# Performance work log

Hardware: AMD Instinct MI355X
Metric: run time of the kernel (lower is better)

## Reference

```python
import jax, jax.numpy as jnp
import numpy as np


def setup_inputs() -> dict:
    key = jax.random.key(0)
    k1, k2, k3, k4, k5 = jax.random.split(key, 5)
    B, T, H, E, F = 4, 2048, 2048, 8, 1024
    s_h = 1.0 / np.sqrt(H)
    s_f = 1.0 / np.sqrt(F)
    return {
        "hidden_states": jax.random.normal(k1, (B, T, H), dtype=jnp.float32),
        "W_router": jax.random.normal(k2, (H, E), dtype=jnp.float32) * s_h,
        "W_gate": jax.random.normal(k3, (E, H, F), dtype=jnp.float32) * s_h,
        "W_up": jax.random.normal(k4, (E, H, F), dtype=jnp.float32) * s_h,
        "W_down": jax.random.normal(k5, (E, F, H), dtype=jnp.float32) * s_f,
    }


def reference(hidden_states, W_router, W_gate, W_up, W_down):
    B, T, H = hidden_states.shape
    E = W_router.shape[1]
    x = hidden_states.reshape(-1, H)  # [N, H]
    # ReMoE router: linear -> ReLU, non-negative weights per expert
    weights = jax.nn.relu(x @ W_router)  # [N, E]
    # Per-expert SwiGLU FFN applied to all tokens; zero-weight experts
    # contribute exactly zero, matching the original masked dispatch.
    gate = jnp.einsum('nh,ehf->enf', x, W_gate)  # [E, N, F]
    up = jnp.einsum('nh,ehf->enf', x, W_up)      # [E, N, F]
    hid = jax.nn.silu(gate) * up                 # [E, N, F]
    expert_out = jnp.einsum('enf,efh->enh', hid, W_down)  # [E, N, H]
    out_flat = jnp.einsum('ne,enh->nh', weights, expert_out)  # [N, H]
    out = out_flat.reshape(B, T, H)
    router_weights = weights.reshape(B, T, E)
    return (out, router_weights)
```

## Files before the change

### kernel.cpp

```cpp
#include <hip/hip_runtime.h>
#include <hip/hip_bf16.h>

#define N_TOK 8192
#define HD    2048
#define NE    8
#define FF    1024

using f32x4  = __attribute__((ext_vector_type(4))) float;
using bf16x8 = __attribute__((ext_vector_type(8))) __bf16;

__device__ __forceinline__ unsigned short f2bf(float f) {
  unsigned u = __float_as_uint(f);
  u += 0x7FFFu + ((u >> 16) & 1u);
  return (unsigned short)(u >> 16);
}

__device__ __forceinline__ void gl_lds16(const void* g, void* l) {
  __builtin_amdgcn_global_load_lds((__attribute__((address_space(1))) void*)g,
                                   (__attribute__((address_space(3))) void*)l,
                                   16, 0, 0);
}

#define WAIT8_BAR() do {                                      \
    asm volatile("s_waitcnt vmcnt(8)" ::: "memory");          \
    __builtin_amdgcn_s_barrier();                             \
    __builtin_amdgcn_sched_barrier(0);                        \
  } while (0)

__global__ void k_tconv(const float* __restrict__ in, unsigned short* __restrict__ out,
                        int R, int C, size_t in_z, size_t out_z, size_t ostride) {
  __shared__ float tile[32][33];
  const int z = blockIdx.z;
  const int c0 = blockIdx.x * 32, r0 = blockIdx.y * 32;
  const int tx = threadIdx.x, ty = threadIdx.y;
  const float* ip = in + (size_t)z * in_z;
  unsigned short* op = out + (size_t)z * out_z;
  #pragma unroll
  for (int i = ty; i < 32; i += 8)
    tile[i][tx] = ip[(size_t)(r0 + i) * C + (c0 + tx)];
  __syncthreads();
  #pragma unroll
  for (int i = ty; i < 32; i += 8)
    op[(size_t)(c0 + i) * ostride + (r0 + tx)] = f2bf(tile[tx][i]);
}

__global__ void k_router(const float* __restrict__ x, const float* __restrict__ Wr,
                         float* __restrict__ w, float* __restrict__ rout,
                         unsigned short* __restrict__ xb) {
  const int lane = threadIdx.x & 63, wv = threadIdx.x >> 6;
  const int n = blockIdx.x * 4 + wv;
  const float* xr = x + (size_t)n * HD + lane * 32;
  unsigned short* xbr = xb + (size_t)n * HD + lane * 32;
  const float* wbase = Wr + (size_t)lane * 32 * NE;
  float acc[8];
  #pragma unroll
  for (int e = 0; e < 8; ++e) acc[e] = 0.f;
  #pragma unroll
  for (int kk = 0; kk < 32; kk += 4) {
    float4 xv = *reinterpret_cast<const float4*>(xr + kk);
    ushort4 o;
    o.x = f2bf(xv.x); o.y = f2bf(xv.y); o.z = f2bf(xv.z); o.w = f2bf(xv.w);
    *reinterpret_cast<ushort4*>(xbr + kk) = o;
    #pragma unroll
    for (int t = 0; t < 4; ++t) {
      const float* wrow = wbase + (kk + t) * 8;
      float4 w0 = *reinterpret_cast<const float4*>(wrow);
      float4 w1 = *reinterpret_cast<const float4*>(wrow + 4);
      float xs = (t == 0) ? xv.x : (t == 1) ? xv.y : (t == 2) ? xv.z : xv.w;
      acc[0] += xs * w0.x; acc[1] += xs * w0.y; acc[2] += xs * w0.z; acc[3] += xs * w0.w;
      acc[4] += xs * w1.x; acc[5] += xs * w1.y; acc[6] += xs * w1.z; acc[7] += xs * w1.w;
    }
  }
  #pragma unroll
  for (int off = 32; off; off >>= 1) {
    #pragma unroll
    for (int e = 0; e < 8; ++e) acc[e] += __shfl_down(acc[e], off);
  }
  if (lane == 0) {
    #pragma unroll
    for (int e = 0; e < 8; ++e) {
      float v = acc[e] > 0.f ? acc[e] : 0.f;
      w[n * 8 + e] = v;
      rout[n * 8 + e] = v;
    }
  }
}

__global__ void k_compact(const float* __restrict__ w, int* __restrict__ idx,
                          int* __restrict__ cnt) {
  const int e = blockIdx.x;
  __shared__ int base;
  __shared__ int scan[4];
  if (threadIdx.x == 0) base = 0;
  __syncthreads();
  const int lane = threadIdx.x & 63, wvi = threadIdx.x >> 6;
  for (int c0 = 0; c0 < N_TOK; c0 += 256) {
    const int n = c0 + threadIdx.x;
    const bool act = w[n * 8 + e] > 0.f;
    unsigned long long m = __ballot(act);
    const int pre  = __popcll(m & ((1ull << lane) - 1ull));
    if (lane == 0) scan[wvi] = __popcll(m);
    __syncthreads();
    int woff = 0;
    #pragma unroll
    for (int i = 0; i < 4; ++i) if (i < wvi) woff += scan[i];
    const int tot = scan[0] + scan[1] + scan[2] + scan[3];
    if (act) idx[e * N_TOK + base + woff + pre] = n;
    __syncthreads();
    if (threadIdx.x == 0) base += tot;
    __syncthreads();
  }
  const int M = base;
  if (threadIdx.x == 0) cnt[e] = M;
  const int Mpad = (M + 255) & ~255;
  for (int i = M + threadIdx.x; i < Mpad; i += 256) idx[e * N_TOK + i] = 0;
}

#define G1_MFMA(accM, barr) do {                                                 \
    __builtin_amdgcn_s_setprio(1);                                               \
    _Pragma("unroll")                                                            \
    for (int i = 0; i < 4; ++i) {                                                \
      _Pragma("unroll")                                                          \
      for (int j = 0; j < 4; ++j)                                                \
        accM[i][j] = __builtin_amdgcn_mfma_f32_16x16x32_bf16(av_[i], (barr)[j], accM[i][j], 0,0,0); \
    }                                                                            \
    __builtin_amdgcn_s_setprio(0);                                               \
  } while (0)

#define G1_ST_A(koff, base) do {                                                 \
    gl_lds16(aP0 + (koff), (base) + wv * 1024);                                  \
    gl_lds16(aP1 + (koff), (base) + (wv + 8) * 1024);                            \
  } while (0)
#define G1_ST_B(koff, bgb, bub) do {                                             \
    gl_lds16(gBg + bOff + (koff), (bgb) + wv * 1024);                            \
    gl_lds16(gBu + bOff + (koff), (bub) + wv * 1024);                            \
  } while (0)

#define G1_HALF(rsl, hh, ISSUE_B) do {                                           \
    const char* Ab_ = As  + (rsl) * 32768 + (hh) * 16384 + aoff;                 \
    const char* Bg_ = Bgs + (rsl) * 16384 + (hh) * 8192 + boff;                  \
    const char* Bu_ = Bus + (rsl) * 16384 + (hh) * 8192 + boff;                  \
    bf16x8 av_[4], bb_[4];                                                       \
    _Pragma("unroll")                                                            \
    for (int i = 0; i < 4; ++i) av_[i] = *(const bf16x8*)(Ab_ + i * 1024);       \
    _Pragma("unroll")                                                            \
    for (int j = 0; j < 4; ++j) bb_[j] = *(const bf16x8*)(Bg_ + j * 1024);       \
    G1_MFMA(ag, bb_);                                                            \
    ISSUE_B;                                                                     \
    _Pragma("unroll")                                                            \
    for (int j = 0; j < 4; ++j) bb_[j] = *(const bf16x8*)(Bu_ + j * 1024);       \
    G1_MFMA(au, bb_);                                                            \
  } while (0)

__global__ void __launch_bounds__(512, 2) k_gemm1(
    const unsigned short* __restrict__ xb,
    const unsigned short* __restrict__ Wg,
    const unsigned short* __restrict__ Wu,
    const float* __restrict__ w,
    const int* __restrict__ idx,
    const int* __restrict__ cnt,
    unsigned short* __restrict__ A2,
    int e0, int k2g, int nwg) {
  extern __shared__ char lds[];
  char* As  = lds;
  char* Bgs = lds + 65536;
  char* Bus = lds + 98304;
  const int tid = threadIdx.x;
  const int l = tid & 63, wv = tid >> 6;

  const int h = blockIdx.x;
  const int chunk = nwg >> 3;
  const int L = (h & 7) * chunk + (h >> 3);
  const int eloc = L >> 8;
  const int e = e0 + eloc;
  const int idxq = L & 255;
  const int sub = idxq >> 5;
  const int f = ((sub & 1) << 2) | ((idxq >> 3) & 3);
  const int y = ((sub >> 1) << 3) | (idxq & 7);
  const int bm = y << 8;
  const int bf = f << 7;
  const int wr = wv >> 1, wc = wv & 1;

  const int Me = cnt[e];
  if (bm >= Me) return;
  const int* idxe = idx + e * N_TOK;

  const unsigned short* gBg = Wg + ((size_t)e * FF + bf) * HD;
  const unsigned short* gBu = Wu + ((size_t)e * FF + bf) * HD;

  const int scolE = (((l & 3) ^ ((l >> 3) & 3)) << 3);
  const int fr  = l & 15;
  const int cph = (((l >> 4) ^ ((fr >> 1) & 3)) << 4);
  const int aoff = (wr * 64 + fr) * 64 + cph;
  const int boff = (wc * 64 + fr) * 64 + cph;

  const unsigned short* aP0 = xb + (size_t)idxe[bm + wv * 16 + (l >> 2)] * HD + scolE;
  const unsigned short* aP1 = xb + (size_t)idxe[bm + (wv + 8) * 16 + (l >> 2)] * HD + scolE;
  const size_t bOff = (size_t)(wv * 16 + (l >> 2)) * HD + scolE;

  f32x4 ag[4][4], au[4][4];
  const f32x4 zero = {0.f, 0.f, 0.f, 0.f};
  #pragma unroll
  for (int i = 0; i < 4; ++i) {
    #pragma unroll
    for (int j = 0; j < 4; ++j) { ag[i][j] = zero; au[i][j] = zero; }
  }

  G1_ST_A(0,  As);
  G1_ST_B(0,  Bgs, Bus);
  G1_ST_A(32, As + 16384);
  G1_ST_B(32, Bgs + 8192, Bus + 8192);
  G1_ST_A(64, As + 32768);
  G1_ST_B(64, Bgs + 16384, Bus + 16384);
  WAIT8_BAR();

  const int NT = HD / 64;
  for (int t = 0; t < NT; ++t) {
    const int rs = t & 1, sw = rs ^ 1;
    const int kn1 = ((t + 1 < NT) ? t + 1 : NT - 1) * 64;
    const int kn2 = ((t + 2 < NT) ? t + 2 : NT - 1) * 64;
    G1_ST_A(kn1 + 32, As + sw * 32768 + 16384);
    G1_HALF(rs, 0, G1_ST_B(kn1 + 32, Bgs + sw * 16384 + 8192, Bus + sw * 16384 + 8192));
    WAIT8_BAR();
    G1_ST_A(kn2, As + rs * 32768);
    G1_HALF(rs, 1, G1_ST_B(kn2, Bgs + rs * 16384, Bus + rs * 16384));
    WAIT8_BAR();
  }

  const int orow = (l >> 4) << 2;
  #pragma unroll
  for (int am = 0; am < 4; ++am) {
    #pragma unroll
    for (int rr = 0; rr < 4; ++rr) {
      const int cm = bm + wr * 64 + am * 16 + orow + rr;
      const int n = idxe[cm];
      const float wn = w[n * 8 + e];
      size_t obase = (size_t)n * k2g + (size_t)eloc * FF + bf + wc * 64 + fr;
      #pragma unroll
      for (int j = 0; j < 4; ++j) {
        const float g = ag[am][j][rr];
        const float u = au[am][j][rr];
        const float s = g / (1.f + __expf(-g));
        A2[obase + j * 16] = f2bf(s * u * wn);
      }
    }
  }
}

#define G2_ST_A(koff, base) do {                                                 \
    gl_lds16(gA + aOff0 + (koff), (base) + wv * 1024);                           \
    gl_lds16(gA + aOff1 + (koff), (base) + (wv + 8) * 1024);                     \
  } while (0)
#define G2_ST_B(koff, base) do {                                                 \
    gl_lds16(gB + bOff0 + (koff), (base) + wv * 1024);                           \
    gl_lds16(gB + bOff1 + (koff), (base) + (wv + 8) * 1024);                     \
  } while (0)

#define G2_HALF(rsl, hh, ISSUE_B) do {                                           \
    const char* Ab_ = As + (rsl) * 32768 + (hh) * 16384 + aoff;                  \
    const char* Bb_ = Bs + (rsl) * 32768 + (hh) * 16384 + boff;                  \
    bf16x8 av_[8], bv_[4];                                                       \
    _Pragma("unroll")                                                            \
    for (int i = 0; i < 8; ++i) av_[i] = *(const bf16x8*)(Ab_ + i * 1024);       \
    _Pragma("unroll")                                                            \
    for (int j = 0; j < 4; ++j) bv_[j] = *(const bf16x8*)(Bb_ + j * 1024);       \
    __builtin_amdgcn_s_setprio(1);                                               \
    _Pragma("unroll")                                                            \
    for (int i = 0; i < 4; ++i) {                                                \
      _Pragma("unroll")                                                          \
      for (int j = 0; j < 4; ++j)                                                \
        acc[i][j] = __builtin_amdgcn_mfma_f32_16x16x32_bf16(av_[i], bv_[j], acc[i][j], 0,0,0); \
    }                                                                            \
    __builtin_amdgcn_s_setprio(0);                                               \
    ISSUE_B;                                                                     \
    __builtin_amdgcn_s_setprio(1);                                               \
    _Pragma("unroll")                                                            \
    for (int i = 4; i < 8; ++i) {                                                \
      _Pragma("unroll")                                                          \
      for (int j = 0; j < 4; ++j)                                                \
        acc[i][j] = __builtin_amdgcn_mfma_f32_16x16x32_bf16(av_[i], bv_[j], acc[i][j], 0,0,0); \
    }                                                                            \
    __builtin_amdgcn_s_setprio(0);                                               \
  } while (0)

__global__ void __launch_bounds__(512, 2) k_gemm2(
    const unsigned short* __restrict__ A2,
    const unsigned short* __restrict__ Wd,
    float* __restrict__ out,
    int k2g, int accum) {
  extern __shared__ char lds[];
  char* As = lds;
  char* Bs = lds + 65536;
  const int tid = threadIdx.x;
  const int l = tid & 63, wv = tid >> 6;

  const int h = blockIdx.x;
  const int L = (h & 7) * 32 + (h >> 3);
  const int y = L >> 3;
  const int x = L & 7;
  const int bm = y << 8;
  const int bn = x << 8;
  const int wr = wv >> 2, wc = wv & 3;

  const unsigned short* gA = A2 + (size_t)bm * k2g;
  const unsigned short* gB = Wd + (size_t)bn * (NE * FF);

  const int scolE = (((l & 3) ^ ((l >> 3) & 3)) << 3);
  const int fr  = l & 15;
  const int cph = (((l >> 4) ^ ((fr >> 1) & 3)) << 4);
  const int aoff = (wr * 128 + fr) * 64 + cph;
  const int boff = (wc * 64 + fr) * 64 + cph;

  const size_t aOff0 = (size_t)(wv * 16 + (l >> 2)) * k2g + scolE;
  const size_t aOff1 = (size_t)((wv + 8) * 16 + (l >> 2)) * k2g + scolE;
  const size_t bOff0 = (size_t)(wv * 16 + (l >> 2)) * (NE * FF) + scolE;
  const size_t bOff1 = (size_t)((wv + 8) * 16 + (l >> 2)) * (NE * FF) + scolE;

  f32x4 acc[8][4];
  const f32x4 zero = {0.f, 0.f, 0.f, 0.f};
  #pragma unroll
  for (int i = 0; i < 8; ++i) {
    #pragma unroll
    for (int j = 0; j < 4; ++j) acc[i][j] = zero;
  }

  G2_ST_A(0,  As);
  G2_ST_B(0,  Bs);
  G2_ST_A(32, As + 16384);
  G2_ST_B(32, Bs + 16384);
  G2_ST_A(64, As + 32768);
  G2_ST_B(64, Bs + 32768);
  WAIT8_BAR();

  const int NT = k2g / 64;
  for (int t = 0; t < NT; ++t) {
    const int rs = t & 1, sw = rs ^ 1;
    const int kn1 = ((t + 1 < NT) ? t + 1 : NT - 1) * 64;
    const int kn2 = ((t + 2 < NT) ? t + 2 : NT - 1) * 64;
    G2_ST_A(kn1 + 32, As + sw * 32768 + 16384);
    G2_HALF(rs, 0, G2_ST_B(kn1 + 32, Bs + sw * 32768 + 16384));
    WAIT8_BAR();
    G2_ST_A(kn2, As + rs * 32768);
    G2_HALF(rs, 1, G2_ST_B(kn2, Bs + rs * 32768));
    WAIT8_BAR();
  }

  const int orow = (l >> 4) << 2;
  #pragma unroll
  for (int am = 0; am < 8; ++am) {
    #pragma unroll
    for (int rr = 0; rr < 4; ++rr) {
      const int n = bm + wr * 128 + am * 16 + orow + rr;
      float* op = out + (size_t)n * HD + bn + wc * 64 + fr;
      #pragma unroll
      for (int j = 0; j < 4; ++j) {
        const float v = acc[am][j][rr];
        op[j * 16] = accum ? (op[j * 16] + v) : v;
      }
    }
  }
}

extern "C" void kernel_launch(void* const* d_in, const int* in_sizes, int n_in,
                              void* d_out, int out_size, void* d_ws, size_t ws_size,
                              hipStream_t stream) {
  (void)in_sizes; (void)out_size;
  if (n_in < 5) return;
  const float* x  = (const float*)d_in[0];
  const float* Wr = (const float*)d_in[1];
  const float* Wg = (const float*)d_in[2];
  const float* Wu = (const float*)d_in[3];
  const float* Wd = (const float*)d_in[4];
  float* out  = (float*)d_out;
  float* rout = out + (size_t)N_TOK * HD;

  hipFuncSetAttribute((const void*)k_gemm1, hipFuncAttributeMaxDynamicSharedMemorySize, 131072);
  hipFuncSetAttribute((const void*)k_gemm2, hipFuncAttributeMaxDynamicSharedMemorySize, 131072);

  char* ws = (char*)d_ws;
  const size_t SZ_XB = (size_t)N_TOK * HD * 2;
  const size_t SZ_W  = (size_t)NE * HD * FF * 2;
  unsigned short* xb    = (unsigned short*)(ws);
  unsigned short* Wg_bt = (unsigned short*)(ws + SZ_XB);
  unsigned short* Wu_bt = (unsigned short*)(ws + SZ_XB + SZ_W);
  unsigned short* Wd_bt = (unsigned short*)(ws + SZ_XB + 2 * SZ_W);
  float*          wbuf  = (float*)(ws + SZ_XB + 3 * SZ_W);
  size_t off = SZ_XB + 3 * SZ_W + (size_t)N_TOK * NE * 4;
  int* idxbuf = (int*)(ws + off);  off += (size_t)NE * N_TOK * 4;
  int* cntbuf = (int*)(ws + off);  off += 256;
  const size_t fixed = off;
  unsigned short* A2 = (unsigned short*)(ws + fixed);

  const size_t perE = (size_t)N_TOK * FF * 2;
  int G = 8;
  while (G > 1 && fixed + (size_t)G * perE > ws_size) G >>= 1;

  dim3 tb(32, 8);
  k_tconv<<<dim3(FF / 32, HD / 32, NE), tb, 0, stream>>>(
      Wg, Wg_bt, HD, FF, (size_t)HD * FF, (size_t)FF * HD, (size_t)HD);
  k_tconv<<<dim3(FF / 32, HD / 32, NE), tb, 0, stream>>>(
      Wu, Wu_bt, HD, FF, (size_t)HD * FF, (size_t)FF * HD, (size_t)HD);
  k_tconv<<<dim3(HD / 32, FF / 32, NE), tb, 0, stream>>>(
      Wd, Wd_bt, FF, HD, (size_t)FF * HD, (size_t)FF, (size_t)(NE * FF));

  k_router<<<N_TOK / 4, 256, 0, stream>>>(x, Wr, wbuf, rout, xb);

  k_compact<<<NE, 256, 0, stream>>>(wbuf, idxbuf, cntbuf);

  const int k2g = G * FF;
  for (int e0 = 0; e0 < NE; e0 += G) {
    hipMemsetAsync(A2, 0, (size_t)G * perE, stream);
    const int nwg1 = 256 * G;
    k_gemm1<<<nwg1, 512, 131072, stream>>>(xb, Wg_bt, Wu_bt, wbuf, idxbuf, cntbuf,
                                           A2, e0, k2g, nwg1);
    k_gemm2<<<(N_TOK / 256) * (HD / 256), 512, 131072, stream>>>(
        A2, Wd_bt + (size_t)e0 * FF, out, k2g, e0 != 0);
  }
}
```

Before: 710.3 us.

## Restructure GEMM main loops into 8-phase ping-pong schedule with wave-contiguous LDS staging

Both expert GEMM kernels move from a 3-stage prefetch with half-tile compute to a double-buffered loop split into four phases per K tile. Each phase reads one operand slice from LDS, issues the next global-to-LDS copies, then synchronises and runs a 16-MFMA block. Staging addresses now map each thread to a contiguous tid*16 slot rather than per-wave rows. The aim is to interleave LDS reads, global loads and MFMA work more finely, in the style of ping-pong scheduling. The cost is more barriers per tile and one fewer stage of prefetch depth.

```diff
diff --git a/kernel.cpp b/kernel.cpp
--- a/kernel.cpp
+++ b/kernel.cpp
@@ -9,6 +9,16 @@
 using f32x4  = __attribute__((ext_vector_type(4))) float;
 using bf16x8 = __attribute__((ext_vector_type(8))) __bf16;
 
+#define MFMA16(a, b, c) __builtin_amdgcn_mfma_f32_16x16x32_bf16((a), (b), (c), 0, 0, 0)
+#define BARX() do { __builtin_amdgcn_s_barrier(); __builtin_amdgcn_sched_barrier(0); } while (0)
+#define PH_BAR() do {                                           \
+    __builtin_amdgcn_sched_barrier(0);                          \
+    __builtin_amdgcn_s_barrier();                               \
+    asm volatile("s_waitcnt lgkmcnt(0)" ::: "memory");          \
+    __builtin_amdgcn_sched_barrier(0);                          \
+  } while (0)
+#define VMW4() asm volatile("s_waitcnt vmcnt(4)" ::: "memory")
+
 __device__ __forceinline__ unsigned short f2bf(float f) {
   unsigned u = __float_as_uint(f);
   u += 0x7FFFu + ((u >> 16) & 1u);
@@ -20,12 +30,6 @@
                                    (__attribute__((address_space(3))) void*)l,
                                    16, 0, 0);
 }
-
-#define WAIT8_BAR() do {                                      \
-    asm volatile("s_waitcnt vmcnt(8)" ::: "memory");          \
-    __builtin_amdgcn_s_barrier();                             \
-    __builtin_amdgcn_sched_barrier(0);                        \
-  } while (0)
 
 __global__ void k_tconv(const float* __restrict__ in, unsigned short* __restrict__ out,
                         int R, int C, size_t in_z, size_t out_z, size_t ostride) {
@@ -116,40 +120,33 @@
   for (int i = M + threadIdx.x; i < Mpad; i += 256) idx[e * N_TOK + i] = 0;
 }
 
-#define G1_MFMA(accM, barr) do {                                                 \
+#define G1_STA(kb, kh, d) do {                                                   \
+    gl_lds16(aPs0 + (kb) + (kh) * 32, As + (d) * 32768 + (kh) * 16384 + tid * 16);          \
+    gl_lds16(aPs1 + (kb) + (kh) * 32, As + (d) * 32768 + (kh) * 16384 + 8192 + tid * 16);   \
+  } while (0)
+#define G1_STB(kb, kh, d) do {                                                   \
+    gl_lds16(gBgs + (kb) + (kh) * 32, Bgs + (d) * 16384 + (kh) * 8192 + tid * 16);          \
+    gl_lds16(gBus + (kb) + (kh) * 32, Bus + (d) * 16384 + (kh) * 8192 + tid * 16);          \
+  } while (0)
+#define G1_RDA(kh) do {                                                          \
+    const char* p_ = As + d * 32768 + (kh) * 16384 + arow + cphR;                \
+    av[0] = *(const bf16x8*)(p_);        av[1] = *(const bf16x8*)(p_ + 1024);    \
+    av[2] = *(const bf16x8*)(p_ + 2048); av[3] = *(const bf16x8*)(p_ + 3072);    \
+  } while (0)
+#define G1_RDB(B_, kh) do {                                                      \
+    const char* p_ = (B_) + d * 16384 + (kh) * 8192 + brow + cphR;               \
+    bv[0] = *(const bf16x8*)(p_);        bv[1] = *(const bf16x8*)(p_ + 1024);    \
+    bv[2] = *(const bf16x8*)(p_ + 2048); bv[3] = *(const bf16x8*)(p_ + 3072);    \
+  } while (0)
+#define G1_MMX(ACC) do {                                                         \
     __builtin_amdgcn_s_setprio(1);                                               \
     _Pragma("unroll")                                                            \
-    for (int i = 0; i < 4; ++i) {                                                \
+    for (int m_ = 0; m_ < 4; ++m_) {                                             \
       _Pragma("unroll")                                                          \
-      for (int j = 0; j < 4; ++j)                                                \
-        accM[i][j] = __builtin_amdgcn_mfma_f32_16x16x32_bf16(av_[i], (barr)[j], accM[i][j], 0,0,0); \
+      for (int j_ = 0; j_ < 4; ++j_)                                             \
+        ACC[m_][j_] = MFMA16(av[m_], bv[j_], ACC[m_][j_]);                       \
     }                                                                            \
     __builtin_amdgcn_s_setprio(0);                                               \
-  } while (0)
-
-#define G1_ST_A(koff, base) do {                                                 \
-    gl_lds16(aP0 + (koff), (base) + wv * 1024);                                  \
-    gl_lds16(aP1 + (koff), (base) + (wv + 8) * 1024);                            \
-  } while (0)
-#define G1_ST_B(koff, bgb, bub) do {                                             \
-    gl_lds16(gBg + bOff + (koff), (bgb) + wv * 1024);                            \
-    gl_lds16(gBu + bOff + (koff), (bub) + wv * 1024);                            \
-  } while (0)
-
-#define G1_HALF(rsl, hh, ISSUE_B) do {                                           \
-    const char* Ab_ = As  + (rsl) * 32768 + (hh) * 16384 + aoff;                 \
-    const char* Bg_ = Bgs + (rsl) * 16384 + (hh) * 8192 + boff;                  \
-    const char* Bu_ = Bus + (rsl) * 16384 + (hh) * 8192 + boff;                  \
-    bf16x8 av_[4], bb_[4];                                                       \
-    _Pragma("unroll")                                                            \
-    for (int i = 0; i < 4; ++i) av_[i] = *(const bf16x8*)(Ab_ + i * 1024);       \
-    _Pragma("unroll")                                                            \
-    for (int j = 0; j < 4; ++j) bb_[j] = *(const bf16x8*)(Bg_ + j * 1024);       \
-    G1_MFMA(ag, bb_);                                                            \
-    ISSUE_B;                                                                     \
-    _Pragma("unroll")                                                            \
-    for (int j = 0; j < 4; ++j) bb_[j] = *(const bf16x8*)(Bu_ + j * 1024);       \
-    G1_MFMA(au, bb_);                                                            \
   } while (0)
 
 __global__ void __launch_bounds__(512, 2) k_gemm1(
@@ -188,15 +185,17 @@
   const unsigned short* gBg = Wg + ((size_t)e * FF + bf) * HD;
   const unsigned short* gBu = Wu + ((size_t)e * FF + bf) * HD;
 
-  const int scolE = (((l & 3) ^ ((l >> 3) & 3)) << 3);
-  const int fr  = l & 15;
-  const int cph = (((l >> 4) ^ ((fr >> 1) & 3)) << 4);
-  const int aoff = (wr * 64 + fr) * 64 + cph;
-  const int boff = (wc * 64 + fr) * 64 + cph;
-
-  const unsigned short* aP0 = xb + (size_t)idxe[bm + wv * 16 + (l >> 2)] * HD + scolE;
-  const unsigned short* aP1 = xb + (size_t)idxe[bm + (wv + 8) * 16 + (l >> 2)] * HD + scolE;
-  const size_t bOff = (size_t)(wv * 16 + (l >> 2)) * HD + scolE;
+  const int srow  = tid >> 2;
+  const int scolE = (((tid & 3) ^ ((tid >> 3) & 3)) << 3);
+  const int fr   = l & 15;
+  const int cphR = (((l >> 4) ^ ((fr >> 1) & 3)) << 4);
+  const int arow = (wr * 64 + fr) * 64;
+  const int brow = (wc * 64 + fr) * 64;
+
+  const unsigned short* aPs0 = xb + (size_t)idxe[bm + srow] * HD + scolE;
+  const unsigned short* aPs1 = xb + (size_t)idxe[bm + 128 + srow] * HD + scolE;
+  const unsigned short* gBgs = gBg + (size_t)srow * HD + scolE;
+  const unsigned short* gBus = gBu + (size_t)srow * HD + scolE;
 
   f32x4 ag[4][4], au[4][4];
   const f32x4 zero = {0.f, 0.f, 0.f, 0.f};
@@ -206,25 +205,42 @@
     for (int j = 0; j < 4; ++j) { ag[i][j] = zero; au[i][j] = zero; }
   }
 
-  G1_ST_A(0,  As);
-  G1_ST_B(0,  Bgs, Bus);
-  G1_ST_A(32, As + 16384);
-  G1_ST_B(32, Bgs + 8192, Bus + 8192);
-  G1_ST_A(64, As + 32768);
-  G1_ST_B(64, Bgs + 16384, Bus + 16384);
-  WAIT8_BAR();
+  G1_STA(0, 0, 0);
+  G1_STB(0, 0, 0);
+  G1_STA(0, 1, 0);
+  G1_STB(0, 1, 0);
+  VMW4();
+  BARX();
 
   const int NT = HD / 64;
   for (int t = 0; t < NT; ++t) {
-    const int rs = t & 1, sw = rs ^ 1;
-    const int kn1 = ((t + 1 < NT) ? t + 1 : NT - 1) * 64;
-    const int kn2 = ((t + 2 < NT) ? t + 2 : NT - 1) * 64;
-    G1_ST_A(kn1 + 32, As + sw * 32768 + 16384);
-    G1_HALF(rs, 0, G1_ST_B(kn1 + 32, Bgs + sw * 16384 + 8192, Bus + sw * 16384 + 8192));
-    WAIT8_BAR();
-    G1_ST_A(kn2, As + rs * 32768);
-    G1_HALF(rs, 1, G1_ST_B(kn2, Bgs + rs * 16384, Bus + rs * 16384));
-    WAIT8_BAR();
+    const int d = t & 1, dn = d ^ 1;
+    const int kn = ((t + 1 < NT) ? t + 1 : NT - 1) * 64;
+    bf16x8 av[4], bv[4];
+    G1_RDA(0);
+    G1_RDB(Bgs, 0);
+    G1_STA(kn, 0, dn);
+    PH_BAR();
+    G1_MMX(ag);
+    BARX();
+    G1_RDB(Bus, 0);
+    G1_STB(kn, 0, dn);
+    PH_BAR();
+    G1_MMX(au);
+    VMW4();
+    BARX();
+    G1_RDA(1);
+    G1_RDB(Bgs, 1);
+    G1_STA(kn, 1, dn);
+    PH_BAR();
+    G1_MMX(ag);
+    BARX();
+    G1_RDB(Bus, 1);
+    G1_STB(kn, 1, dn);
+    PH_BAR();
+    G1_MMX(au);
+    VMW4();
+    BARX();
   }
 
   const int orow = (l >> 4) << 2;
@@ -247,38 +263,31 @@
   }
 }
 
-#define G2_ST_A(koff, base) do {                                                 \
-    gl_lds16(gA + aOff0 + (koff), (base) + wv * 1024);                           \
-    gl_lds16(gA + aOff1 + (koff), (base) + (wv + 8) * 1024);                     \
-  } while (0)
-#define G2_ST_B(koff, base) do {                                                 \
-    gl_lds16(gB + bOff0 + (koff), (base) + wv * 1024);                           \
-    gl_lds16(gB + bOff1 + (koff), (base) + (wv + 8) * 1024);                     \
-  } while (0)
-
-#define G2_HALF(rsl, hh, ISSUE_B) do {                                           \
-    const char* Ab_ = As + (rsl) * 32768 + (hh) * 16384 + aoff;                  \
-    const char* Bb_ = Bs + (rsl) * 32768 + (hh) * 16384 + boff;                  \
-    bf16x8 av_[8], bv_[4];                                                       \
-    _Pragma("unroll")                                                            \
-    for (int i = 0; i < 8; ++i) av_[i] = *(const bf16x8*)(Ab_ + i * 1024);       \
-    _Pragma("unroll")                                                            \
-    for (int j = 0; j < 4; ++j) bv_[j] = *(const bf16x8*)(Bb_ + j * 1024);       \
+#define G2_STA(kb, kh, d) do {                                                   \
+    gl_lds16(gAs0 + (kb) + (kh) * 32, As + (d) * 32768 + (kh) * 16384 + tid * 16);          \
+    gl_lds16(gAs1 + (kb) + (kh) * 32, As + (d) * 32768 + (kh) * 16384 + 8192 + tid * 16);   \
+  } while (0)
+#define G2_STB(kb, kh, d) do {                                                   \
+    gl_lds16(gBs0 + (kb) + (kh) * 32, Bs + (d) * 32768 + (kh) * 16384 + tid * 16);          \
+    gl_lds16(gBs1 + (kb) + (kh) * 32, Bs + (d) * 32768 + (kh) * 16384 + 8192 + tid * 16);   \
+  } while (0)
+#define G2_RDA(kh, mb) do {                                                      \
+    const char* p_ = As + d * 32768 + (kh) * 16384 + arow + (mb) * 1024 + cphR;  \
+    av[0] = *(const bf16x8*)(p_);        av[1] = *(const bf16x8*)(p_ + 1024);    \
+    av[2] = *(const bf16x8*)(p_ + 2048); av[3] = *(const bf16x8*)(p_ + 3072);    \
+  } while (0)
+#define G2_RDB(kh) do {                                                          \
+    const char* p_ = Bs + d * 32768 + (kh) * 16384 + brow + cphR;                \
+    bv[0] = *(const bf16x8*)(p_);        bv[1] = *(const bf16x8*)(p_ + 1024);    \
+    bv[2] = *(const bf16x8*)(p_ + 2048); bv[3] = *(const bf16x8*)(p_ + 3072);    \
+  } while (0)
+#define G2_MMX(mb) do {                                                          \
     __builtin_amdgcn_s_setprio(1);                                               \
     _Pragma("unroll")                                                            \
-    for (int i = 0; i < 4; ++i) {                                                \
+    for (int m_ = 0; m_ < 4; ++m_) {                                             \
       _Pragma("unroll")                                                          \
-      for (int j = 0; j < 4; ++j)                                                \
-        acc[i][j] = __builtin_amdgcn_mfma_f32_16x16x32_bf16(av_[i], bv_[j], acc[i][j], 0,0,0); \
-    }                                                                            \
-    __builtin_amdgcn_s_setprio(0);                                               \
-    ISSUE_B;                                                                     \
-    __builtin_amdgcn_s_setprio(1);                                               \
-    _Pragma("unroll")                                                            \
-    for (int i = 4; i < 8; ++i) {                                                \
-      _Pragma("unroll")                                                          \
-      for (int j = 0; j < 4; ++j)                                                \
-        acc[i][j] = __builtin_amdgcn_mfma_f32_16x16x32_bf16(av_[i], bv_[j], acc[i][j], 0,0,0); \
+      for (int j_ = 0; j_ < 4; ++j_)                                             \
+        acc[(mb) + m_][j_] = MFMA16(av[m_], bv[j_], acc[(mb) + m_][j_]);         \
     }                                                                            \
     __builtin_amdgcn_s_setprio(0);                                               \
   } while (0)
@@ -305,16 +314,17 @@
   const unsigned short* gA = A2 + (size_t)bm * k2g;
   const unsigned short* gB = Wd + (size_t)bn * (NE * FF);
 
-  const int scolE = (((l & 3) ^ ((l >> 3) & 3)) << 3);
-  const int fr  = l & 15;
-  const int cph = (((l >> 4) ^ ((fr >> 1) & 3)) << 4);
-  const int aoff = (wr * 128 + fr) * 64 + cph;
-  const int boff = (wc * 64 + fr) * 64 + cph;
-
-  const size_t aOff0 = (size_t)(wv * 16 + (l >> 2)) * k2g + scolE;
-  const size_t aOff1 = (size_t)((wv + 8) * 16 + (l >> 2)) * k2g + scolE;
-  const size_t bOff0 = (size_t)(wv * 16 + (l >> 2)) * (NE * FF) + scolE;
-  const size_t bOff1 = (size_t)((wv + 8) * 16 + (l >> 2)) * (NE * FF) + scolE;
+  const int srow  = tid >> 2;
+  const int scolE = (((tid & 3) ^ ((tid >> 3) & 3)) << 3);
+  const int fr   = l & 15;
+  const int cphR = (((l >> 4) ^ ((fr >> 1) & 3)) << 4);
+  const int arow = (wr * 128 + fr) * 64;
+  const int brow = (wc * 64 + fr) * 64;
+
+  const unsigned short* gAs0 = gA + (size_t)srow * k2g + scolE;
+  const unsigned short* gAs1 = gA + (size_t)(srow + 128) * k2g + scolE;
+  const unsigned short* gBs0 = gB + (size_t)srow * (NE * FF) + scolE;
+  const unsigned short* gBs1 = gB + (size_t)(srow + 128) * (NE * FF) + scolE;
 
   f32x4 acc[8][4];
   const f32x4 zero = {0.f, 0.f, 0.f, 0.f};
@@ -324,25 +334,42 @@
     for (int j = 0; j < 4; ++j) acc[i][j] = zero;
   }
 
-  G2_ST_A(0,  As);
-  G2_ST_B(0,  Bs);
-  G2_ST_A(32, As + 16384);
-  G2_ST_B(32, Bs + 16384);
-  G2_ST_A(64, As + 32768);
-  G2_ST_B(64, Bs + 32768);
-  WAIT8_BAR();
+  G2_STA(0, 0, 0);
+  G2_STB(0, 0, 0);
+  G2_STA(0, 1, 0);
+  G2_STB(0, 1, 0);
+  VMW4();
+  BARX();
 
   const int NT = k2g / 64;
   for (int t = 0; t < NT; ++t) {
-    const int rs = t & 1, sw = rs ^ 1;
-    const int kn1 = ((t + 1 < NT) ? t + 1 : NT - 1) * 64;
-    const int kn2 = ((t + 2 < NT) ? t + 2 : NT - 1) * 64;
-    G2_ST_A(kn1 + 32, As + sw * 32768 + 16384);
-    G2_HALF(rs, 0, G2_ST_B(kn1 + 32, Bs + sw * 32768 + 16384));
-    WAIT8_BAR();
-    G2_ST_A(kn2, As + rs * 32768);
-    G2_HALF(rs, 1, G2_ST_B(kn2, Bs + rs * 32768));
-    WAIT8_BAR();
+    const int d = t & 1, dn = d ^ 1;
+    const int kn = ((t + 1 < NT) ? t + 1 : NT - 1) * 64;
+    bf16x8 av[4], bv[4];
+    G2_RDA(0, 0);
+    G2_RDB(0);
+    G2_STA(kn, 0, dn);
+    PH_BAR();
+    G2_MMX(0);
+    BARX();
+    G2_RDA(0, 4);
+    G2_STB(kn, 0, dn);
+    PH_BAR();
+    G2_MMX(4);
+    VMW4();
+    BARX();
+    G2_RDA(1, 0);
+    G2_RDB(1);
+    G2_STA(kn, 1, dn);
+    PH_BAR();
+    G2_MMX(0);
+    BARX();
+    G2_RDA(1, 4);
+    G2_STB(kn, 1, dn);
+    PH_BAR();
+    G2_MMX(4);
+    VMW4();
+    BARX();
   }
 
   const int orow = (l >> 4) << 2;
```

New measurement: 712.5 us. Within noise of the previous version (+0.3%).
